# Optimization experiments

Hardware: AMD Instinct MI355X
Metric: run time of the kernel (lower is better)

Reference implementation:

```python
import jax, jax.numpy as jnp
import numpy as np

B, CIN, SEQ, H, W = 16, 8, 32, 128, 128
COUT, K = 8, 3


def setup_inputs() -> dict:
    key = jax.random.key(0)
    k1, k2, k3 = jax.random.split(key, 3)
    X = jax.random.normal(k1, (B, CIN, SEQ, H, W), dtype=jnp.float32)
    # single gate conv: [4*Cout, Cin+Cout, K, K]
    Wc = jax.random.normal(k2, (4 * COUT, CIN + COUT, K, K), dtype=jnp.float32) * 0.05
    bc = jax.random.normal(k3, (4 * COUT,), dtype=jnp.float32) * 0.05
    return {"X": X, "Wc": Wc, "bc": bc}


def reference(X, Wc, bc):
    # X: (B, Cin, S, H, W) -> cell_output: (B, Cout, S, H, W)
    Bb, Cin, S, Hh, Ww = X.shape
    Cout = Wc.shape[0] // 4
    h0 = jnp.zeros((Bb, Cout, Hh, Ww), X.dtype)
    c0 = jnp.zeros_like(h0)
    Xt = jnp.moveaxis(X, 2, 0)  # (S, B, Cin, H, W) for scan over time

    def step(carry, x):
        h, c = carry
        z = jax.lax.conv_general_dilated(
            jnp.concatenate([x, h], axis=1), Wc,
            window_strides=(1, 1), padding=((1, 1), (1, 1)),
            dimension_numbers=("NCHW", "OIHW", "NCHW"),
        ) + bc[None, :, None, None]
        i, f, g, o = jnp.split(z, 4, axis=1)
        c_new = jax.nn.sigmoid(f) * c + jax.nn.sigmoid(i) * jnp.tanh(g)
        h_new = jax.nn.sigmoid(o) * jnp.tanh(c_new)
        return (h_new, c_new), h_new

    _, hs = jax.lax.scan(step, (h0, c0), Xt)  # hs: (S, B, Cout, H, W)
    return jnp.moveaxis(hs, 0, 2)  # (B, Cout, S, H, W)
```

## Files before the change

kernel.cpp:

```cpp
#include <hip/hip_runtime.h>

#define SEQ   32
#define HH    128
#define WW    128
#define CINC  8
#define COUTC 8
#define NG    32
#define ICH   16
#define TAPS  9
#define ROWS  4
#define COLS  130

typedef _Float16 half8 __attribute__((ext_vector_type(8)));
typedef _Float16 half4 __attribute__((ext_vector_type(4)));
typedef float floatx16 __attribute__((ext_vector_type(16)));

__device__ __forceinline__ float fast_rcp(float x) { return __builtin_amdgcn_rcpf(x); }
__device__ __forceinline__ float sigmoidf_(float x) {
    return fast_rcp(1.0f + __expf(-x));
}
__device__ __forceinline__ float tanhf_(float x) {
    float e = __expf(-2.0f * x);
    return (1.0f - e) * fast_rcp(1.0f + e);
}

__global__ void prep_weights(const float* __restrict__ Wc, _Float16* __restrict__ Wf,
                             unsigned* __restrict__ flags) {
    int i = blockIdx.x * 256 + threadIdx.x;
    if (i < 1024) flags[i] = 0u;
    if (i >= TAPS * NG * ICH) return;
    int tap = i / (NG * ICH);
    int r   = i % (NG * ICH);
    int g   = r >> 4;
    int ch  = r & 15;
    int half = ch >> 3, c8 = ch & 7;
    int ky = tap / 3, kx = tap % 3;
    float w = Wc[g * (ICH * 9) + ch * 9 + ky * 3 + kx];
    Wf[((tap * NG + g) * 2 + half) * 8 + c8] = (_Float16)w;
}

__device__ __forceinline__ void stage_X(const float* __restrict__ X, int b, int y0, int tt,
                                        int tid, _Float16* ldsH, _Float16* ldsL) {
#pragma unroll
    for (int i = 0; i < 3; ++i) {
        int idx = tid + i * 256;
        if (idx >= ROWS * COLS) break;
        int col = idx % COLS;
        int row = idx / COLS;
        int gy = y0 + row - 1;
        int gx = col - 1;
        bool inb = ((unsigned)gy < HH) && ((unsigned)gx < WW);
        float v[8];
#pragma unroll
        for (int j = 0; j < 8; ++j)
            v[j] = inb ? X[(((size_t)(b * CINC + j) * SEQ + tt) * HH + gy) * WW + gx] : 0.0f;
        union { half8 h; float4 f; } uh, ul;
#pragma unroll
        for (int j = 0; j < 8; ++j) {
            _Float16 hi = (_Float16)v[j];
            uh.h[j] = hi;
            ul.h[j] = (_Float16)(v[j] - (float)hi);
        }
        *(float4*)&ldsH[(size_t)idx * 8] = uh.f;
        *(float4*)&ldsL[(size_t)idx * 8] = ul.f;
    }
}

__device__ __forceinline__ void stage_halo(const float* __restrict__ out, int b, int gy,
                                           int t, int ldsrow, int lane,
                                           _Float16* ldsH, _Float16* ldsL) {
    for (int col = lane; col < COLS; col += 64) {
        int gx = col - 1;
        bool inb = ((unsigned)gy < HH) && ((unsigned)gx < WW);
        float v[8];
#pragma unroll
        for (int j = 0; j < 8; ++j)
            v[j] = inb ? __hip_atomic_load(
                             &out[(((size_t)(b * COUTC + j) * SEQ + (t - 1)) * HH + gy) * WW + gx],
                             __ATOMIC_RELAXED, __HIP_MEMORY_SCOPE_AGENT)
                       : 0.0f;
        union { half8 h; float4 f; } uh, ul;
#pragma unroll
        for (int j = 0; j < 8; ++j) {
            _Float16 hi = (_Float16)v[j];
            uh.h[j] = hi;
            ul.h[j] = (_Float16)(v[j] - (float)hi);
        }
        int item = ROWS * COLS + ldsrow * COLS + col;
        *(float4*)&ldsH[(size_t)item * 8] = uh.f;
        *(float4*)&ldsL[(size_t)item * 8] = ul.f;
    }
}

template <int T0, int T1>
__device__ __forceinline__ void do_taps(int ry, int x0, int lg, int lh,
                                        const half8* wfrag,
                                        const _Float16* ldsH, const _Float16* ldsL,
                                        floatx16& acc0, floatx16& acc1) {
#pragma unroll
    for (int tap = T0; tap < T1; ++tap) {
        int ky = tap / 3, kx = tap % 3;
        int row = ry + ky;
        int base0 = ((lh * ROWS + row) * COLS + (x0 + lg + kx)) * 8;
        int base1 = base0 + 32 * 8;
        half8 bh0 = *(const half8*)&ldsH[base0];
        half8 bl0 = *(const half8*)&ldsL[base0];
        half8 bh1 = *(const half8*)&ldsH[base1];
        half8 bl1 = *(const half8*)&ldsL[base1];
        acc0 = __builtin_amdgcn_mfma_f32_32x32x16_f16(wfrag[tap], bh0, acc0, 0, 0, 0);
        acc1 = __builtin_amdgcn_mfma_f32_32x32x16_f16(wfrag[tap], bh1, acc1, 0, 0, 0);
        acc0 = __builtin_amdgcn_mfma_f32_32x32x16_f16(wfrag[tap], bl0, acc0, 0, 0, 0);
        acc1 = __builtin_amdgcn_mfma_f32_32x32x16_f16(wfrag[tap], bl1, acc1, 0, 0, 0);
    }
}

__global__ __launch_bounds__(256, 4) void lstm_fused(
    const float* __restrict__ X,
    const _Float16* __restrict__ Wf,
    const float* __restrict__ bc,
    float* __restrict__ out,
    unsigned* __restrict__ flags)
{
    __shared__ __align__(16) _Float16 ldsH[2 * ROWS * COLS * 8];
    __shared__ __align__(16) _Float16 ldsL[2 * ROWS * COLS * 8];

    const int tid = threadIdx.x;
    const int blk = blockIdx.x;
    const int b   = blk >> 6;
    const int yb  = blk & 63;
    const int y0  = yb * 2;

    const int lane = tid & 63;
    const int w    = tid >> 6;
    const int lg   = lane & 31;
    const int lh   = lane >> 5;

    const bool hasUp = (yb > 0);
    const bool hasDn = (yb < 63);

    half8 wfrag[TAPS];
#pragma unroll
    for (int tap = 0; tap < TAPS; ++tap)
        wfrag[tap] = *(const half8*)&Wf[((tap * NG + lg) * 2 + lh) * 8];

    float bi[4], bf4[4], bg[4], bo[4];
#pragma unroll
    for (int r = 0; r < 4; ++r) {
        int oc = r + 4 * lh;
        bi[r]  = bc[oc];
        bf4[r] = bc[oc + 8];
        bg[r]  = bc[oc + 16];
        bo[r]  = bc[oc + 24];
    }

    float creg[8];
#pragma unroll
    for (int r = 0; r < 8; ++r) creg[r] = 0.0f;

    const int ry = w >> 1;
    const int x0 = (w & 1) * 64;
    const int y  = y0 + ry;

#pragma unroll
    for (int i = 0; i < 3; ++i) {
        int idx = tid + i * 256;
        if (idx >= ROWS * COLS) break;
        int item = ROWS * COLS + idx;
        *(float4*)&ldsH[(size_t)item * 8] = float4{0.f, 0.f, 0.f, 0.f};
        *(float4*)&ldsL[(size_t)item * 8] = float4{0.f, 0.f, 0.f, 0.f};
    }
    stage_X(X, b, y0, 0, tid, ldsH, ldsL);
    __syncthreads();

    for (int t = 0; t < SEQ; ++t) {
        floatx16 acc0, acc1;
#pragma unroll
        for (int r = 0; r < 16; ++r) { acc0[r] = 0.0f; acc1[r] = 0.0f; }

        if (w == 0) {
            if (t > 0) {
                if (hasUp && lane == 0) {
                    int polls = 0;
                    while (__hip_atomic_fetch_add(&flags[blk - 1], 0u, __ATOMIC_RELAXED,
                                                  __HIP_MEMORY_SCOPE_AGENT) < (unsigned)t
                           && ++polls < (1 << 17))
                        __builtin_amdgcn_s_sleep(1);
                }
                asm volatile("" ::: "memory");
                stage_halo(out, b, y0 - 1, t, 0, lane, ldsH, ldsL);
            }
        } else if (w == 1) {
            if (t > 0) {
                if (hasDn && lane == 0) {
                    int polls = 0;
                    while (__hip_atomic_fetch_add(&flags[blk + 1], 0u, __ATOMIC_RELAXED,
                                                  __HIP_MEMORY_SCOPE_AGENT) < (unsigned)t
                           && ++polls < (1 << 17))
                        __builtin_amdgcn_s_sleep(1);
                }
                asm volatile("" ::: "memory");
                stage_halo(out, b, y0 + 2, t, 3, lane, ldsH, ldsL);
            }
        } else {
            do_taps<0, 6>(ry, x0, lg, lh, wfrag, ldsH, ldsL, acc0, acc1);
        }
        __syncthreads();

        if (ry == 0)
            do_taps<0, 9>(ry, x0, lg, lh, wfrag, ldsH, ldsL, acc0, acc1);
        else
            do_taps<6, 9>(ry, x0, lg, lh, wfrag, ldsH, ldsL, acc0, acc1);
        __syncthreads();

#pragma unroll
        for (int tl = 0; tl < 2; ++tl) {
            floatx16 A = tl ? acc1 : acc0;
            int px = x0 + tl * 32 + lg;
            half4 hh, hl;
#pragma unroll
            for (int r = 0; r < 4; ++r) {
                int oc = r + 4 * lh;
                float zi = A[r]      + bi[r];
                float zf = A[4 + r]  + bf4[r];
                float zg = A[8 + r]  + bg[r];
                float zo = A[12 + r] + bo[r];
                float cp = creg[tl * 4 + r];
                float cn = sigmoidf_(zf) * cp + sigmoidf_(zi) * tanhf_(zg);
                creg[tl * 4 + r] = cn;
                float hval = sigmoidf_(zo) * tanhf_(cn);
                __hip_atomic_store(
                    &out[(((size_t)(b * COUTC + oc) * SEQ + t) * HH + y) * WW + px],
                    hval, __ATOMIC_RELAXED, __HIP_MEMORY_SCOPE_AGENT);
                _Float16 hi = (_Float16)hval;
                hh[r] = hi;
                hl[r] = (_Float16)(hval - (float)hi);
            }
            int hbase = (((1 * ROWS) + 1 + ry) * COLS + (px + 1)) * 8 + 4 * lh;
            *(half4*)&ldsH[hbase] = hh;
            *(half4*)&ldsL[hbase] = hl;
        }

        __syncthreads();
        if (tid == 0 && t + 1 < SEQ)
            __hip_atomic_fetch_add(&flags[blk], 1u,
                                   __ATOMIC_RELAXED, __HIP_MEMORY_SCOPE_AGENT);

        if (t + 1 < SEQ)
            stage_X(X, b, y0, t + 1, tid, ldsH, ldsL);
        __syncthreads();
    }
}

__global__ __launch_bounds__(256, 4) void step_kernel(
    const float* __restrict__ X,
    const _Float16* __restrict__ Wf,
    const float* __restrict__ bc,
    float* __restrict__ out,
    float* __restrict__ c,
    int t)
{
    __shared__ __align__(16) _Float16 ldsH[2 * ROWS * COLS * 8];
    __shared__ __align__(16) _Float16 ldsL[2 * ROWS * COLS * 8];

    const int tid = threadIdx.x;
    const int b   = blockIdx.x >> 6;
    const int y0  = (blockIdx.x & 63) * 2;

    for (int idx = tid; idx < 2 * ROWS * COLS; idx += 256) {
        int col  = idx % COLS;
        int tmp  = idx / COLS;
        int half = tmp >> 2;
        int row  = tmp & 3;
        int gy = y0 + row - 1;
        int gx = col - 1;
        bool inb = ((unsigned)gy < HH) && ((unsigned)gx < WW);
        float v[8];
#pragma unroll
        for (int j = 0; j < 8; ++j) {
            int ch = half * 8 + j;
            float val = 0.0f;
            if (inb) {
                if (ch < CINC)
                    val = X[(((size_t)(b * CINC + ch) * SEQ + t) * HH + gy) * WW + gx];
                else if (t > 0)
                    val = out[(((size_t)(b * COUTC + (ch - 8)) * SEQ + (t - 1)) * HH + gy) * WW + gx];
            }
            v[j] = val;
        }
        union { half8 h; float4 f; } uh, ul;
#pragma unroll
        for (int j = 0; j < 8; ++j) {
            _Float16 hi = (_Float16)v[j];
            uh.h[j] = hi;
            ul.h[j] = (_Float16)(v[j] - (float)hi);
        }
        *(float4*)&ldsH[(size_t)idx * 8] = uh.f;
        *(float4*)&ldsL[(size_t)idx * 8] = ul.f;
    }

    const int lane = tid & 63;
    const int w    = tid >> 6;
    const int lg   = lane & 31;
    const int lh   = lane >> 5;

    half8 wfrag[TAPS];
#pragma unroll
    for (int tap = 0; tap < TAPS; ++tap)
        wfrag[tap] = *(const half8*)&Wf[((tap * NG + lg) * 2 + lh) * 8];

    __syncthreads();

    const int ry = w >> 1;
    const int x0 = (w & 1) * 64;

    floatx16 acc0, acc1;
#pragma unroll
    for (int r = 0; r < 16; ++r) { acc0[r] = 0.0f; acc1[r] = 0.0f; }

#pragma unroll
    for (int tap = 0; tap < TAPS; ++tap) {
        int ky = tap / 3, kx = tap % 3;
        int row = ry + ky;
        int base0 = ((lh * ROWS + row) * COLS + (x0 + lg + kx)) * 8;
        int base1 = base0 + 32 * 8;
        half8 bh0 = *(const half8*)&ldsH[base0];
        half8 bl0 = *(const half8*)&ldsL[base0];
        half8 bh1 = *(const half8*)&ldsH[base1];
        half8 bl1 = *(const half8*)&ldsL[base1];
        acc0 = __builtin_amdgcn_mfma_f32_32x32x16_f16(wfrag[tap], bh0, acc0, 0, 0, 0);
        acc1 = __builtin_amdgcn_mfma_f32_32x32x16_f16(wfrag[tap], bh1, acc1, 0, 0, 0);
        acc0 = __builtin_amdgcn_mfma_f32_32x32x16_f16(wfrag[tap], bl0, acc0, 0, 0, 0);
        acc1 = __builtin_amdgcn_mfma_f32_32x32x16_f16(wfrag[tap], bl1, acc1, 0, 0, 0);
    }

    const int y = y0 + ry;
#pragma unroll
    for (int tl = 0; tl < 2; ++tl) {
        floatx16 A = tl ? acc1 : acc0;
        int px = x0 + tl * 32 + lg;
#pragma unroll
        for (int r = 0; r < 4; ++r) {
            int oc = r + 4 * lh;
            float zi = A[r]      + bc[oc];
            float zf = A[4 + r]  + bc[oc + 8];
            float zg = A[8 + r]  + bc[oc + 16];
            float zo = A[12 + r] + bc[oc + 24];
            size_t ci = ((size_t)(b * COUTC + oc) * HH + y) * WW + px;
            float cp = (t > 0) ? c[ci] : 0.0f;
            float cn = sigmoidf_(zf) * cp + sigmoidf_(zi) * tanhf_(zg);
            c[ci] = cn;
            out[(((size_t)(b * COUTC + oc) * SEQ + t) * HH + y) * WW + px]
                = sigmoidf_(zo) * tanhf_(cn);
        }
    }
}

extern "C" void kernel_launch(void* const* d_in, const int* in_sizes, int n_in,
                              void* d_out, int out_size, void* d_ws, size_t ws_size,
                              hipStream_t stream) {
    const float* X  = (const float*)d_in[0];
    const float* Wc = (const float*)d_in[1];
    const float* bc = (const float*)d_in[2];
    float* out = (float*)d_out;

    _Float16* Wf    = (_Float16*)d_ws;
    unsigned* flags = (unsigned*)((char*)d_ws + 12288);

    prep_weights<<<18, 256, 0, stream>>>(Wc, Wf, flags);

    void* args[] = { (void*)&X, (void*)&Wf, (void*)&bc, (void*)&out, (void*)&flags };
    hipError_t err = hipLaunchCooperativeKernel((const void*)lstm_fused,
                                                dim3(16 * 64), dim3(256),
                                                args, 0, stream);
    if (err != hipSuccess) {
        float* c = (float*)((char*)d_ws + 16384);
        for (int t = 0; t < SEQ; ++t) {
            step_kernel<<<16 * 64, 256, 0, stream>>>(X, Wf, bc, out, c, t);
        }
    }
}
```

Measured before the change: 964.2 us.

## Prefetch next X into registers, overlap interior taps with halo wait, pad flags

The global loads of the next timestep's input are now issued at the top of the loop into registers and written to LDS only at the end, which hides their latency behind compute. Every wave computes the taps that do not need the neighbour halo before the spin-wait. After the wait, all 256 threads cooperatively load the halo rows, instead of two waves loading them while the others compute. The per-block flags are padded to separate cache lines to avoid false sharing, and the spin sleep interval and poll limit change. One barrier is removed. The cost is extra register pressure from the 24 prefetched floats under launch bounds of 4 blocks per CU.

```diff
diff --git a/kernel.cpp b/kernel.cpp
--- a/kernel.cpp
+++ b/kernel.cpp
@@ -10,6 +10,7 @@
 #define TAPS  9
 #define ROWS  4
 #define COLS  130
+#define FSTRIDE 32
 
 typedef _Float16 half8 __attribute__((ext_vector_type(8)));
 typedef _Float16 half4 __attribute__((ext_vector_type(4)));
@@ -27,7 +28,7 @@
 __global__ void prep_weights(const float* __restrict__ Wc, _Float16* __restrict__ Wf,
                              unsigned* __restrict__ flags) {
     int i = blockIdx.x * 256 + threadIdx.x;
-    if (i < 1024) flags[i] = 0u;
+    if (i < 1024) flags[i * FSTRIDE] = 0u;
     if (i >= TAPS * NG * ICH) return;
     int tap = i / (NG * ICH);
     int r   = i % (NG * ICH);
@@ -39,8 +40,16 @@
     Wf[((tap * NG + g) * 2 + half) * 8 + c8] = (_Float16)w;
 }
 
-__device__ __forceinline__ void stage_X(const float* __restrict__ X, int b, int y0, int tt,
-                                        int tid, _Float16* ldsH, _Float16* ldsL) {
+__device__ __forceinline__ void spin_wait(unsigned* f, unsigned t) {
+    int polls = 0;
+    while (__hip_atomic_fetch_add(f, 0u, __ATOMIC_RELAXED,
+                                  __HIP_MEMORY_SCOPE_AGENT) < t
+           && ++polls < (1 << 15))
+        __builtin_amdgcn_s_sleep(4);
+}
+
+__device__ __forceinline__ void stage_X_issue(const float* __restrict__ X, int b, int y0,
+                                              int tt, int tid, float (&v)[3][8]) {
 #pragma unroll
     for (int i = 0; i < 3; ++i) {
         int idx = tid + i * 256;
@@ -50,45 +59,27 @@
         int gy = y0 + row - 1;
         int gx = col - 1;
         bool inb = ((unsigned)gy < HH) && ((unsigned)gx < WW);
-        float v[8];
 #pragma unroll
         for (int j = 0; j < 8; ++j)
-            v[j] = inb ? X[(((size_t)(b * CINC + j) * SEQ + tt) * HH + gy) * WW + gx] : 0.0f;
+            v[i][j] = inb ? X[(((size_t)(b * CINC + j) * SEQ + tt) * HH + gy) * WW + gx] : 0.0f;
+    }
+}
+
+__device__ __forceinline__ void stage_X_write(int tid, const float (&v)[3][8],
+                                              _Float16* ldsH, _Float16* ldsL) {
+#pragma unroll
+    for (int i = 0; i < 3; ++i) {
+        int idx = tid + i * 256;
+        if (idx >= ROWS * COLS) break;
         union { half8 h; float4 f; } uh, ul;
 #pragma unroll
         for (int j = 0; j < 8; ++j) {
-            _Float16 hi = (_Float16)v[j];
+            _Float16 hi = (_Float16)v[i][j];
             uh.h[j] = hi;
-            ul.h[j] = (_Float16)(v[j] - (float)hi);
+            ul.h[j] = (_Float16)(v[i][j] - (float)hi);
         }
         *(float4*)&ldsH[(size_t)idx * 8] = uh.f;
         *(float4*)&ldsL[(size_t)idx * 8] = ul.f;
-    }
-}
-
-__device__ __forceinline__ void stage_halo(const float* __restrict__ out, int b, int gy,
-                                           int t, int ldsrow, int lane,
-                                           _Float16* ldsH, _Float16* ldsL) {
-    for (int col = lane; col < COLS; col += 64) {
-        int gx = col - 1;
-        bool inb = ((unsigned)gy < HH) && ((unsigned)gx < WW);
-        float v[8];
-#pragma unroll
-        for (int j = 0; j < 8; ++j)
-            v[j] = inb ? __hip_atomic_load(
-                             &out[(((size_t)(b * COUTC + j) * SEQ + (t - 1)) * HH + gy) * WW + gx],
-                             __ATOMIC_RELAXED, __HIP_MEMORY_SCOPE_AGENT)
-                       : 0.0f;
-        union { half8 h; float4 f; } uh, ul;
-#pragma unroll
-        for (int j = 0; j < 8; ++j) {
-            _Float16 hi = (_Float16)v[j];
-            uh.h[j] = hi;
-            ul.h[j] = (_Float16)(v[j] - (float)hi);
-        }
-        int item = ROWS * COLS + ldsrow * COLS + col;
-        *(float4*)&ldsH[(size_t)item * 8] = uh.f;
-        *(float4*)&ldsL[(size_t)item * 8] = ul.f;
     }
 }
 
@@ -169,48 +160,68 @@
         *(float4*)&ldsH[(size_t)item * 8] = float4{0.f, 0.f, 0.f, 0.f};
         *(float4*)&ldsL[(size_t)item * 8] = float4{0.f, 0.f, 0.f, 0.f};
     }
-    stage_X(X, b, y0, 0, tid, ldsH, ldsL);
+    {
+        float v0[3][8];
+        stage_X_issue(X, b, y0, 0, tid, v0);
+        stage_X_write(tid, v0, ldsH, ldsL);
+    }
     __syncthreads();
 
     for (int t = 0; t < SEQ; ++t) {
+        float xreg[3][8];
+        if (t + 1 < SEQ)
+            stage_X_issue(X, b, y0, t + 1, tid, xreg);
+
         floatx16 acc0, acc1;
 #pragma unroll
         for (int r = 0; r < 16; ++r) { acc0[r] = 0.0f; acc1[r] = 0.0f; }
 
-        if (w == 0) {
-            if (t > 0) {
-                if (hasUp && lane == 0) {
-                    int polls = 0;
-                    while (__hip_atomic_fetch_add(&flags[blk - 1], 0u, __ATOMIC_RELAXED,
-                                                  __HIP_MEMORY_SCOPE_AGENT) < (unsigned)t
-                           && ++polls < (1 << 17))
-                        __builtin_amdgcn_s_sleep(1);
+        if (ry == 0)
+            do_taps<3, 9>(ry, x0, lg, lh, wfrag, ldsH, ldsL, acc0, acc1);
+        else
+            do_taps<0, 6>(ry, x0, lg, lh, wfrag, ldsH, ldsL, acc0, acc1);
+
+        if (t > 0) {
+            if (w == 0 && lane == 0 && hasUp)
+                spin_wait(&flags[(blk - 1) * FSTRIDE], (unsigned)t);
+            if (w == 1 && lane == 0 && hasDn)
+                spin_wait(&flags[(blk + 1) * FSTRIDE], (unsigned)t);
+        }
+        __syncthreads();
+
+        if (t > 0) {
+            for (int idx = tid; idx < 2 * COLS; idx += 256) {
+                int bot    = (idx >= COLS);
+                int col    = idx - bot * COLS;
+                int gy     = bot ? (y0 + 2) : (y0 - 1);
+                int ldsrow = bot ? 3 : 0;
+                int gx = col - 1;
+                bool inb = ((unsigned)gy < HH) && ((unsigned)gx < WW);
+                float v[8];
+#pragma unroll
+                for (int j = 0; j < 8; ++j)
+                    v[j] = inb ? __hip_atomic_load(
+                                     &out[(((size_t)(b * COUTC + j) * SEQ + (t - 1)) * HH + gy) * WW + gx],
+                                     __ATOMIC_RELAXED, __HIP_MEMORY_SCOPE_AGENT)
+                               : 0.0f;
+                union { half8 h; float4 f; } uh, ul;
+#pragma unroll
+                for (int j = 0; j < 8; ++j) {
+                    _Float16 hi = (_Float16)v[j];
+                    uh.h[j] = hi;
+                    ul.h[j] = (_Float16)(v[j] - (float)hi);
                 }
-                asm volatile("" ::: "memory");
-                stage_halo(out, b, y0 - 1, t, 0, lane, ldsH, ldsL);
+                int item = ROWS * COLS + ldsrow * COLS + col;
+                *(float4*)&ldsH[(size_t)item * 8] = uh.f;
+                *(float4*)&ldsL[(size_t)item * 8] = ul.f;
             }
-        } else if (w == 1) {
-            if (t > 0) {
-                if (hasDn && lane == 0) {
-                    int polls = 0;
-                    while (__hip_atomic_fetch_add(&flags[blk + 1], 0u, __ATOMIC_RELAXED,
-                                                  __HIP_MEMORY_SCOPE_AGENT) < (unsigned)t
-                           && ++polls < (1 << 17))
-                        __builtin_amdgcn_s_sleep(1);
-                }
-                asm volatile("" ::: "memory");
-                stage_halo(out, b, y0 + 2, t, 3, lane, ldsH, ldsL);
-            }
-        } else {
-            do_taps<0, 6>(ry, x0, lg, lh, wfrag, ldsH, ldsL, acc0, acc1);
         }
         __syncthreads();
 
         if (ry == 0)
-            do_taps<0, 9>(ry, x0, lg, lh, wfrag, ldsH, ldsL, acc0, acc1);
+            do_taps<0, 3>(ry, x0, lg, lh, wfrag, ldsH, ldsL, acc0, acc1);
         else
             do_taps<6, 9>(ry, x0, lg, lh, wfrag, ldsH, ldsL, acc0, acc1);
-        __syncthreads();
 
 #pragma unroll
         for (int tl = 0; tl < 2; ++tl) {
@@ -242,11 +253,11 @@
 
         __syncthreads();
         if (tid == 0 && t + 1 < SEQ)
-            __hip_atomic_fetch_add(&flags[blk], 1u,
+            __hip_atomic_fetch_add(&flags[blk * FSTRIDE], 1u,
                                    __ATOMIC_RELAXED, __HIP_MEMORY_SCOPE_AGENT);
 
         if (t + 1 < SEQ)
-            stage_X(X, b, y0, t + 1, tid, ldsH, ldsL);
+            stage_X_write(tid, xreg, ldsH, ldsL);
         __syncthreads();
     }
 }
@@ -364,7 +375,7 @@
     float* out = (float*)d_out;
 
     _Float16* Wf    = (_Float16*)d_ws;
-    unsigned* flags = (unsigned*)((char*)d_ws + 12288);
+    unsigned* flags = (unsigned*)((char*)d_ws + 16384);
 
     prep_weights<<<18, 256, 0, stream>>>(Wc, Wf, flags);
 
@@ -373,7 +384,7 @@
                                                 dim3(16 * 64), dim3(256),
                                                 args, 0, stream);
     if (err != hipSuccess) {
-        float* c = (float*)((char*)d_ws + 16384);
+        float* c = (float*)((char*)d_ws + 16384 + 131072);
         for (int t = 0; t < SEQ; ++t) {
             step_kernel<<<16 * 64, 256, 0, stream>>>(X, Wf, bc, out, c, t);
         }
```

New measurement: 1.247 ms. 1.29x slower.
